# Kernel optimization log

Measured on AMD Instinct MI355X. Metric: run time of the kernel, lower is better.

Reference implementation:

```python
import jax, jax.numpy as jnp
import numpy as np

B, TQ, TK, D, H = 2, 2048, 2048, 1024, 16


def setup_inputs() -> dict:
    key = jax.random.key(0)
    ks = jax.random.split(key, 8)
    s = 1.0 / np.sqrt(D)
    x_q = jax.random.normal(ks[0], (B, TQ, D), jnp.float32)
    x_k = jax.random.normal(ks[1], (B, TK, D), jnp.float32)
    x_v = jax.random.normal(ks[2], (B, TK, D), jnp.float32)
    # causal mask, True = masked (matches masked_fill semantics)
    causal = jnp.triu(jnp.ones((TQ, TK), jnp.bool_), k=1)
    attn_mask = jnp.broadcast_to(causal, (B, TQ, TK))
    Wq = jax.random.normal(ks[3], (D, D), jnp.float32) * s
    Wk = jax.random.normal(ks[4], (D, D), jnp.float32) * s
    Wv = jax.random.normal(ks[5], (D, D), jnp.float32) * s
    Wo = jax.random.normal(ks[6], (D, D), jnp.float32) * s
    z = jnp.zeros((D,), jnp.float32)
    return {"x_q": x_q, "x_k": x_k, "x_v": x_v, "attn_mask": attn_mask,
            "Wq": Wq, "bq": z, "Wk": Wk, "bk": z, "Wv": Wv, "bv": z,
            "Wo": Wo, "bo": z, "n_heads": H}


def reference(x_q, x_k, x_v, attn_mask, Wq, bq, Wk, bk, Wv, bv, Wo, bo, n_heads):
    Bv, Tq, Dm = x_q.shape
    Tk = x_k.shape[1]
    dh = Dm // n_heads
    # nn.Linear: y = x @ W^T + b; split heads -> [B, H, T, dh]
    Q = (jnp.einsum('btd,od->bto', x_q, Wq) + bq).reshape(Bv, Tq, n_heads, dh).transpose(0, 2, 1, 3)
    K = (jnp.einsum('btd,od->bto', x_k, Wk) + bk).reshape(Bv, Tk, n_heads, dh).transpose(0, 2, 1, 3)
    V = (jnp.einsum('btd,od->bto', x_v, Wv) + bv).reshape(Bv, Tk, n_heads, dh).transpose(0, 2, 1, 3)
    scale = 1.0 / np.sqrt(dh).astype(np.float32)
    scores = jnp.einsum('bhqd,bhkd->bhqk', Q, K) * scale  # [B,H,Tq,Tk]
    scores = jnp.where(attn_mask[:, None, :, :], -jnp.inf, scores)
    A = jax.nn.softmax(scores, axis=-1)  # dropout p=0.0 -> identity
    out = jnp.einsum('bhqk,bhkd->bhqd', A, V)
    out = out.transpose(0, 2, 1, 3).reshape(Bv, Tq, Dm)
    return jnp.einsum('btd,od->bto', out, Wo) + bo
```

## Files before the change

### kernel.cpp

```cpp
#include <hip/hip_runtime.h>


typedef __attribute__((ext_vector_type(8))) __bf16 bf16x8;
typedef __attribute__((ext_vector_type(4))) float f32x4;
typedef unsigned short u16;

constexpr int BATCH  = 2;
constexpr int TSEQ   = 2048;
constexpr int DMODEL = 1024;
constexpr int NHEAD  = 16;
constexpr int DHEAD  = 64;
constexpr int MROWS  = BATCH * TSEQ;

static __device__ __forceinline__ u16 f2bf(float f) {
  union { float f; unsigned int u; } v; v.f = f;
  unsigned int u = v.u;
  return (u16)((u + 0x7fffu + ((u >> 16) & 1u)) >> 16);
}

static __device__ __forceinline__ void gload16(const void* g, void* l) {
  __builtin_amdgcn_global_load_lds(
      (const __attribute__((address_space(1))) void*)g,
      (__attribute__((address_space(3))) void*)l, 16, 0, 0);
}

__global__ __launch_bounds__(256) void cvt_multi(const float* __restrict__ s0,
                                                 const float* __restrict__ s1,
                                                 const float* __restrict__ s2,
                                                 const float* __restrict__ s3,
                                                 u16* __restrict__ d0, u16* __restrict__ d1,
                                                 u16* __restrict__ d2, u16* __restrict__ d3,
                                                 int n4) {
  const float* s; u16* d;
  switch (blockIdx.y) {
    case 0: s = s0; d = d0; break;
    case 1: s = s1; d = d1; break;
    case 2: s = s2; d = d2; break;
    default: s = s3; d = d3; break;
  }
  int i = blockIdx.x * 256 + threadIdx.x;
  if (i >= n4) return;
  float4 f = ((const float4*)s)[i];
  ushort4 o;
  o.x = f2bf(f.x); o.y = f2bf(f.y); o.z = f2bf(f.z); o.w = f2bf(f.w);
  ((ushort4*)d)[i] = o;
}

template <typename Epi>
static __device__ __forceinline__ void gemm_body8(const u16* __restrict__ X_,
                                                  const u16* __restrict__ W_,
                                                  const float* __restrict__ bias,
                                                  Epi epi) {
  __shared__ __align__(16) u16 As[2][4096];
  __shared__ __align__(16) u16 Bs[2][4096];
  const int lane = threadIdx.x & 63, wave = threadIdx.x >> 6;
  const int l16 = lane & 15, lk = lane >> 4;
  const int wm = wave >> 2, wn = wave & 3;
  const int row0 = blockIdx.x * 128, col0 = blockIdx.y * 128;
  constexpr int K = DMODEL;
  const u16* ga = X_ + (size_t)(row0 + wave * 16 + l16) * K + lk * 8;
  const u16* gb = W_ + (size_t)(col0 + wave * 16 + l16) * K + lk * 8;
  f32x4 acc[4][2];
#pragma unroll
  for (int mt = 0; mt < 4; ++mt)
#pragma unroll
    for (int nt = 0; nt < 2; ++nt) acc[mt][nt] = (f32x4){0.f, 0.f, 0.f, 0.f};
  gload16(ga, &As[0][wave * 512]);
  gload16(gb, &Bs[0][wave * 512]);
  __syncthreads();
  int buf = 0;
  for (int ks = 0; ks < K / 32; ++ks) {
    if (ks + 1 < K / 32) {
      gload16(ga + (ks + 1) * 32, &As[buf ^ 1][wave * 512]);
      gload16(gb + (ks + 1) * 32, &Bs[buf ^ 1][wave * 512]);
    }
    bf16x8 a[4], b[2];
#pragma unroll
    for (int mt = 0; mt < 4; ++mt)
      a[mt] = *(const bf16x8*)&As[buf][(wm * 4 + mt) * 512 + lane * 8];
#pragma unroll
    for (int nt = 0; nt < 2; ++nt)
      b[nt] = *(const bf16x8*)&Bs[buf][(wn * 2 + nt) * 512 + lane * 8];
#pragma unroll
    for (int mt = 0; mt < 4; ++mt)
#pragma unroll
      for (int nt = 0; nt < 2; ++nt)
        acc[mt][nt] =
            __builtin_amdgcn_mfma_f32_16x16x32_bf16(a[mt], b[nt], acc[mt][nt], 0, 0, 0);
    __syncthreads();
    buf ^= 1;
  }
#pragma unroll
  for (int mt = 0; mt < 4; ++mt)
#pragma unroll
    for (int nt = 0; nt < 2; ++nt)
#pragma unroll
      for (int r = 0; r < 4; ++r) {
        int m = row0 + wm * 64 + mt * 16 + lk * 4 + r;
        int n = col0 + wn * 32 + nt * 16 + l16;
        float v = acc[mt][nt][r] + bias[n];
        epi(m, n, v);
      }
}

template <typename Epi>
static __device__ __forceinline__ void gemm_body4(const u16* __restrict__ X_,
                                                  const u16* __restrict__ W_,
                                                  const float* __restrict__ bias,
                                                  Epi epi) {
  constexpr int K = DMODEL;
  __shared__ __align__(16) u16 As[2][8 * 512];
  __shared__ __align__(16) u16 Bs[2][4 * 512];
  const int lane = threadIdx.x & 63, wave = threadIdx.x >> 6;
  const int l16 = lane & 15, lk = lane >> 4;
  const int wm = wave >> 1, wn = wave & 1;
  const int row0 = blockIdx.x * 128, col0 = blockIdx.y * 64;
  const u16* ga = X_ + (size_t)(row0 + l16) * K + lk * 8;
  const u16* gb = W_ + (size_t)(col0 + l16) * K + lk * 8;
  f32x4 acc[4][2];
#pragma unroll
  for (int mt = 0; mt < 4; ++mt)
#pragma unroll
    for (int nt = 0; nt < 2; ++nt) acc[mt][nt] = (f32x4){0.f, 0.f, 0.f, 0.f};
  auto stage = [&](int bufi, int ks) {
#pragma unroll
    for (int j = 0; j < 2; ++j) {
      int s = j * 4 + wave;
      gload16(ga + (size_t)s * 16 * K + ks * 32, &As[bufi][s * 512]);
    }
    gload16(gb + (size_t)wave * 16 * K + ks * 32, &Bs[bufi][wave * 512]);
  };
  stage(0, 0);
  __syncthreads();
  int buf = 0;
  for (int ks = 0; ks < K / 32; ++ks) {
    if (ks + 1 < K / 32) stage(buf ^ 1, ks + 1);
    bf16x8 a[4], b[2];
#pragma unroll
    for (int mt = 0; mt < 4; ++mt)
      a[mt] = *(const bf16x8*)&As[buf][(wm * 4 + mt) * 512 + lane * 8];
#pragma unroll
    for (int nt = 0; nt < 2; ++nt)
      b[nt] = *(const bf16x8*)&Bs[buf][(wn * 2 + nt) * 512 + lane * 8];
#pragma unroll
    for (int mt = 0; mt < 4; ++mt)
#pragma unroll
      for (int nt = 0; nt < 2; ++nt)
        acc[mt][nt] =
            __builtin_amdgcn_mfma_f32_16x16x32_bf16(a[mt], b[nt], acc[mt][nt], 0, 0, 0);
    __syncthreads();
    buf ^= 1;
  }
#pragma unroll
  for (int mt = 0; mt < 4; ++mt)
#pragma unroll
    for (int nt = 0; nt < 2; ++nt)
#pragma unroll
      for (int r = 0; r < 4; ++r) {
        int m = row0 + wm * 64 + mt * 16 + lk * 4 + r;
        int n = col0 + wn * 32 + nt * 16 + l16;
        float v = acc[mt][nt][r] + bias[n];
        epi(m, n, v);
      }
}

__global__ __launch_bounds__(512) void gemm_qkv(
    const u16* __restrict__ xq, const u16* __restrict__ xk, const u16* __restrict__ xv,
    const u16* __restrict__ wq, const u16* __restrict__ wk, const u16* __restrict__ wv,
    const float* __restrict__ bq, const float* __restrict__ bk, const float* __restrict__ bv,
    u16* __restrict__ Qh, u16* __restrict__ Kh, u16* __restrict__ Vt) {
  const int z = blockIdx.z;
  const u16* X = z == 0 ? xq : (z == 1 ? xk : xv);
  const u16* W = z == 0 ? wq : (z == 1 ? wk : wv);
  const float* bias = z == 0 ? bq : (z == 1 ? bk : bv);
  u16* O01 = z == 0 ? Qh : Kh;
  gemm_body8(X, W, bias, [&](int m, int n, float v) {
    int bb = m >> 11, t = m & (TSEQ - 1);
    int h = n >> 6, dd = n & (DHEAD - 1);
    if (z == 0) v *= 0.18033688011112042f;
    if (z == 2)
      Vt[(((size_t)(bb * NHEAD + h)) * DHEAD + dd) * TSEQ + t] = f2bf(v);
    else
      O01[(((size_t)(bb * NHEAD + h)) * TSEQ + t) * DHEAD + dd] = f2bf(v);
  });
}

__global__ __launch_bounds__(256, 4) void gemm_o(const u16* __restrict__ AO,
                                                 const u16* __restrict__ wo,
                                                 const float* __restrict__ bias,
                                                 float* __restrict__ out) {
  gemm_body4(AO, wo, bias,
             [&](int m, int n, float v) { out[(size_t)m * DMODEL + n] = v; });
}

__global__ __launch_bounds__(512, 6) void flash_attn(const u16* __restrict__ Qh,
                                                     const u16* __restrict__ Kh,
                                                     const u16* __restrict__ Vt,
                                                     u16* __restrict__ AO) {
  const int lane = threadIdx.x & 63, wave = threadIdx.x >> 6;
  const int l16 = lane & 15, lk = lane >> 4;
  const int bh = blockIdx.x;
  const int qt = (gridDim.y - 1) - blockIdx.y;
  const int q0 = qt * 128;
  const int b = bh >> 4, h = bh & 15;

  __shared__ __align__(16) u16 Kl[2][4096];
  __shared__ __align__(16) u16 Vl[2][4096];
  __shared__ __align__(16) u16 plds[8][16][72];

  const u16* Qb = Qh + (size_t)bh * TSEQ * DHEAD;
  const u16* Kb = Kh + (size_t)bh * TSEQ * DHEAD;
  const u16* Vb = Vt + (size_t)bh * DHEAD * TSEQ;

  bf16x8 qf[2];
  {
    const u16* qp = Qb + (size_t)(q0 + wave * 16 + l16) * DHEAD + lk * 8;
    qf[0] = *(const bf16x8*)(qp);
    qf[1] = *(const bf16x8*)(qp + 32);
  }

  float mrow[4], lsum[4];
  f32x4 acco[4];
#pragma unroll
  for (int r = 0; r < 4; ++r) { mrow[r] = -1e30f; lsum[r] = 0.f; }
#pragma unroll
  for (int dt = 0; dt < 4; ++dt) acco[dt] = (f32x4){0.f, 0.f, 0.f, 0.f};

  auto stage_kv = [&](int bufi, int kbase) {
    int trow = (wave >> 1) * 16 + l16;
    int dhs = (wave & 1) * 4 + lk;
    gload16(Kb + (size_t)(kbase + trow) * DHEAD + dhs * 8, &Kl[bufi][wave * 512]);
    gload16(Vb + (size_t)trow * TSEQ + kbase + dhs * 8, &Vl[bufi][wave * 512]);
  };

  const int nkb = 2 * qt + 2;
  const int kbdiag = 2 * qt + (wave >> 2);
  stage_kv(0, 0);
  __syncthreads();
  int buf = 0;
  const int qrow_base = q0 + wave * 16 + 4 * lk;

  for (int kb = 0; kb < nkb; ++kb) {
    const int kbase = kb * 64;
    if (kb + 1 < nkb) stage_kv(buf ^ 1, kbase + 64);

    if (kb <= kbdiag) {
      f32x4 s[4];
#pragma unroll
      for (int nt = 0; nt < 4; ++nt) {
        bf16x8 k0f = *(const bf16x8*)&Kl[buf][nt * 1024 + lane * 8];
        bf16x8 k1f = *(const bf16x8*)&Kl[buf][nt * 1024 + 512 + lane * 8];
        f32x4 z = (f32x4){0.f, 0.f, 0.f, 0.f};
        z = __builtin_amdgcn_mfma_f32_16x16x32_bf16(qf[0], k0f, z, 0, 0, 0);
        z = __builtin_amdgcn_mfma_f32_16x16x32_bf16(qf[1], k1f, z, 0, 0, 0);
        s[nt] = z;
      }
      if (kb == kbdiag) {
#pragma unroll
        for (int nt = 0; nt < 4; ++nt)
#pragma unroll
          for (int r = 0; r < 4; ++r) {
            int kcol = kbase + nt * 16 + l16;
            s[nt][r] = (kcol <= qrow_base + r) ? s[nt][r] : -1e30f;
          }
      }
      float pmax[4];
      bool need = false;
#pragma unroll
      for (int r = 0; r < 4; ++r) {
        pmax[r] = fmaxf(fmaxf(s[0][r], s[1][r]), fmaxf(s[2][r], s[3][r]));
        need |= (pmax[r] > mrow[r] + 12.f);
      }
      if (__any(need)) {
#pragma unroll
        for (int r = 0; r < 4; ++r) {
          float mx = pmax[r];
#pragma unroll
          for (int off = 1; off < 16; off <<= 1) mx = fmaxf(mx, __shfl_xor(mx, off, 16));
          float mnew = fmaxf(mrow[r], mx);
          float alpha = exp2f(mrow[r] - mnew);
          lsum[r] *= alpha;
#pragma unroll
          for (int dt = 0; dt < 4; ++dt) acco[dt][r] *= alpha;
          mrow[r] = mnew;
        }
      }
#pragma unroll
      for (int r = 0; r < 4; ++r)
#pragma unroll
        for (int nt = 0; nt < 4; ++nt) {
          float p = exp2f(s[nt][r] - mrow[r]);
          s[nt][r] = p;
          lsum[r] += p;
        }
#pragma unroll
      for (int nt = 0; nt < 4; ++nt)
#pragma unroll
        for (int r = 0; r < 4; ++r)
          plds[wave][4 * lk + r][nt * 16 + l16] = f2bf(s[nt][r]);
      bf16x8 pf0 = *(const bf16x8*)&plds[wave][l16][lk * 8];
      bf16x8 pf1 = *(const bf16x8*)&plds[wave][l16][32 + lk * 8];
#pragma unroll
      for (int dt = 0; dt < 4; ++dt) {
        bf16x8 v0 = *(const bf16x8*)&Vl[buf][dt * 1024 + lane * 8];
        bf16x8 v1 = *(const bf16x8*)&Vl[buf][dt * 1024 + 512 + lane * 8];
        acco[dt] = __builtin_amdgcn_mfma_f32_16x16x32_bf16(pf0, v0, acco[dt], 0, 0, 0);
        acco[dt] = __builtin_amdgcn_mfma_f32_16x16x32_bf16(pf1, v1, acco[dt], 0, 0, 0);
      }
    }
    __syncthreads();
    buf ^= 1;
  }

#pragma unroll
  for (int r = 0; r < 4; ++r) {
    float t = lsum[r];
#pragma unroll
    for (int off = 1; off < 16; off <<= 1) t += __shfl_xor(t, off, 16);
    lsum[r] = 1.f / t;
  }
#pragma unroll
  for (int dt = 0; dt < 4; ++dt)
#pragma unroll
    for (int r = 0; r < 4; ++r) {
      int t = qrow_base + r;
      int col = h * DHEAD + dt * 16 + l16;
      AO[((size_t)(b * TSEQ + t)) * DMODEL + col] = f2bf(acco[dt][r] * lsum[r]);
    }
}

extern "C" void kernel_launch(void* const* d_in, const int* in_sizes, int n_in,
                              void* d_out, int out_size, void* d_ws, size_t ws_size,
                              hipStream_t stream) {
  const float* x_q = (const float*)d_in[0];
  const float* x_k = (const float*)d_in[1];
  const float* x_v = (const float*)d_in[2];
  const float* Wq = (const float*)d_in[4];
  const float* bq = (const float*)d_in[5];
  const float* Wk = (const float*)d_in[6];
  const float* bk = (const float*)d_in[7];
  const float* Wv = (const float*)d_in[8];
  const float* bv = (const float*)d_in[9];
  const float* Wo = (const float*)d_in[10];
  const float* bo = (const float*)d_in[11];

  const size_t nx = (size_t)MROWS * DMODEL;
  const size_t nw = (size_t)DMODEL * DMODEL;
  u16* ws   = (u16*)d_ws;
  u16* xq_b = ws;
  u16* xk_b = xq_b + nx;
  u16* xv_b = xk_b + nx;
  u16* wq_b = xv_b + nx;
  u16* wk_b = wq_b + nw;
  u16* wv_b = wk_b + nw;
  u16* wo_b = wv_b + nw;
  u16* Qh   = wo_b + nw;
  u16* Kh   = Qh + nx;
  u16* Vt   = Kh + nx;
  u16* AO   = Vt + nx;

  const int n4x = (int)(nx / 4), n4w = (int)(nw / 4);
  cvt_multi<<<dim3((n4x + 255) / 256, 3), 256, 0, stream>>>(
      x_q, x_k, x_v, nullptr, xq_b, xk_b, xv_b, nullptr, n4x);
  cvt_multi<<<dim3((n4w + 255) / 256, 4), 256, 0, stream>>>(
      Wq, Wk, Wv, Wo, wq_b, wk_b, wv_b, wo_b, n4w);

  gemm_qkv<<<dim3(MROWS / 128, DMODEL / 128, 3), 512, 0, stream>>>(
      xq_b, xk_b, xv_b, wq_b, wk_b, wv_b, bq, bk, bv, Qh, Kh, Vt);

  flash_attn<<<dim3(BATCH * NHEAD, TSEQ / 128), 512, 0, stream>>>(Qh, Kh, Vt, AO);

  gemm_o<<<dim3(MROWS / 128, DMODEL / 64), 256, 0, stream>>>(AO, wo_b, bo, (float*)d_out);
}
```

Before: 171.6 us.

## Pair causal q-tiles per block for balanced flash attention work

Reworks flash attention so each 4-wave block processes two 64-row query tiles (31-p and p), giving every block the same number of key-block iterations under the causal mask. This replaces the 8-wave 128-row tiles, whose per-block work varied with position and which left half the waves idle on the diagonal block. It trades a larger K/V staging cost per wave and an extra pipeline restart for better load balance and smaller blocks.

```diff
diff --git a/kernel.cpp b/kernel.cpp
--- a/kernel.cpp
+++ b/kernel.cpp
@@ -193,58 +193,60 @@
              [&](int m, int n, float v) { out[(size_t)m * DMODEL + n] = v; });
 }
 
-__global__ __launch_bounds__(512, 6) void flash_attn(const u16* __restrict__ Qh,
-                                                     const u16* __restrict__ Kh,
-                                                     const u16* __restrict__ Vt,
-                                                     u16* __restrict__ AO) {
+__global__ __launch_bounds__(256) void flash_attn(const u16* __restrict__ Qh,
+                                                  const u16* __restrict__ Kh,
+                                                  const u16* __restrict__ Vt,
+                                                  u16* __restrict__ AO) {
   const int lane = threadIdx.x & 63, wave = threadIdx.x >> 6;
   const int l16 = lane & 15, lk = lane >> 4;
   const int bh = blockIdx.x;
-  const int qt = (gridDim.y - 1) - blockIdx.y;
-  const int q0 = qt * 128;
+  const int p = blockIdx.y;
   const int b = bh >> 4, h = bh & 15;
 
   __shared__ __align__(16) u16 Kl[2][4096];
   __shared__ __align__(16) u16 Vl[2][4096];
-  __shared__ __align__(16) u16 plds[8][16][72];
+  __shared__ __align__(16) u16 plds[4][16][72];
 
   const u16* Qb = Qh + (size_t)bh * TSEQ * DHEAD;
   const u16* Kb = Kh + (size_t)bh * TSEQ * DHEAD;
   const u16* Vb = Vt + (size_t)bh * DHEAD * TSEQ;
 
-  bf16x8 qf[2];
-  {
-    const u16* qp = Qb + (size_t)(q0 + wave * 16 + l16) * DHEAD + lk * 8;
-    qf[0] = *(const bf16x8*)(qp);
-    qf[1] = *(const bf16x8*)(qp + 32);
-  }
-
-  float mrow[4], lsum[4];
-  f32x4 acco[4];
-#pragma unroll
-  for (int r = 0; r < 4; ++r) { mrow[r] = -1e30f; lsum[r] = 0.f; }
-#pragma unroll
-  for (int dt = 0; dt < 4; ++dt) acco[dt] = (f32x4){0.f, 0.f, 0.f, 0.f};
-
   auto stage_kv = [&](int bufi, int kbase) {
-    int trow = (wave >> 1) * 16 + l16;
-    int dhs = (wave & 1) * 4 + lk;
-    gload16(Kb + (size_t)(kbase + trow) * DHEAD + dhs * 8, &Kl[bufi][wave * 512]);
-    gload16(Vb + (size_t)trow * TSEQ + kbase + dhs * 8, &Vl[bufi][wave * 512]);
+#pragma unroll
+    for (int j = 0; j < 2; ++j) {
+      int s = j * 4 + wave;
+      int trow = (s >> 1) * 16 + l16;
+      int dhs = (s & 1) * 4 + lk;
+      gload16(Kb + (size_t)(kbase + trow) * DHEAD + dhs * 8, &Kl[bufi][s * 512]);
+      gload16(Vb + (size_t)trow * TSEQ + kbase + dhs * 8, &Vl[bufi][s * 512]);
+    }
   };
 
-  const int nkb = 2 * qt + 2;
-  const int kbdiag = 2 * qt + (wave >> 2);
-  stage_kv(0, 0);
-  __syncthreads();
-  int buf = 0;
-  const int qrow_base = q0 + wave * 16 + 4 * lk;
-
-  for (int kb = 0; kb < nkb; ++kb) {
-    const int kbase = kb * 64;
-    if (kb + 1 < nkb) stage_kv(buf ^ 1, kbase + 64);
-
-    if (kb <= kbdiag) {
+  auto run_tile = [&](int qt) {
+    const int q0 = qt * 64;
+    bf16x8 qf[2];
+    {
+      const u16* qp = Qb + (size_t)(q0 + wave * 16 + l16) * DHEAD + lk * 8;
+      qf[0] = *(const bf16x8*)(qp);
+      qf[1] = *(const bf16x8*)(qp + 32);
+    }
+    float mrow[4], lsum[4];
+    f32x4 acco[4];
+#pragma unroll
+    for (int r = 0; r < 4; ++r) { mrow[r] = -1e30f; lsum[r] = 0.f; }
+#pragma unroll
+    for (int dt = 0; dt < 4; ++dt) acco[dt] = (f32x4){0.f, 0.f, 0.f, 0.f};
+
+    const int qrow_base = q0 + wave * 16 + 4 * lk;
+    const int nkb = qt + 1;
+    stage_kv(0, 0);
+    __syncthreads();
+    int buf = 0;
+
+    for (int kb = 0; kb < nkb; ++kb) {
+      const int kbase = kb * 64;
+      if (kb + 1 < nkb) stage_kv(buf ^ 1, kbase + 64);
+
       f32x4 s[4];
 #pragma unroll
       for (int nt = 0; nt < 4; ++nt) {
@@ -255,7 +257,7 @@
         z = __builtin_amdgcn_mfma_f32_16x16x32_bf16(qf[1], k1f, z, 0, 0, 0);
         s[nt] = z;
       }
-      if (kb == kbdiag) {
+      if (kb == qt) {
 #pragma unroll
         for (int nt = 0; nt < 4; ++nt)
 #pragma unroll
@@ -289,9 +291,9 @@
       for (int r = 0; r < 4; ++r)
 #pragma unroll
         for (int nt = 0; nt < 4; ++nt) {
-          float p = exp2f(s[nt][r] - mrow[r]);
-          s[nt][r] = p;
-          lsum[r] += p;
+          float pv = exp2f(s[nt][r] - mrow[r]);
+          s[nt][r] = pv;
+          lsum[r] += pv;
         }
 #pragma unroll
       for (int nt = 0; nt < 4; ++nt)
@@ -307,26 +309,29 @@
         acco[dt] = __builtin_amdgcn_mfma_f32_16x16x32_bf16(pf0, v0, acco[dt], 0, 0, 0);
         acco[dt] = __builtin_amdgcn_mfma_f32_16x16x32_bf16(pf1, v1, acco[dt], 0, 0, 0);
       }
-    }
-    __syncthreads();
-    buf ^= 1;
-  }
-
-#pragma unroll
-  for (int r = 0; r < 4; ++r) {
-    float t = lsum[r];
-#pragma unroll
-    for (int off = 1; off < 16; off <<= 1) t += __shfl_xor(t, off, 16);
-    lsum[r] = 1.f / t;
-  }
-#pragma unroll
-  for (int dt = 0; dt < 4; ++dt)
+      __syncthreads();
+      buf ^= 1;
+    }
+
 #pragma unroll
     for (int r = 0; r < 4; ++r) {
-      int t = qrow_base + r;
-      int col = h * DHEAD + dt * 16 + l16;
-      AO[((size_t)(b * TSEQ + t)) * DMODEL + col] = f2bf(acco[dt][r] * lsum[r]);
-    }
+      float t = lsum[r];
+#pragma unroll
+      for (int off = 1; off < 16; off <<= 1) t += __shfl_xor(t, off, 16);
+      lsum[r] = 1.f / t;
+    }
+#pragma unroll
+    for (int dt = 0; dt < 4; ++dt)
+#pragma unroll
+      for (int r = 0; r < 4; ++r) {
+        int t = qrow_base + r;
+        int col = h * DHEAD + dt * 16 + l16;
+        AO[((size_t)(b * TSEQ + t)) * DMODEL + col] = f2bf(acco[dt][r] * lsum[r]);
+      }
+  };
+
+  run_tile(31 - p);
+  run_tile(p);
 }
 
 extern "C" void kernel_launch(void* const* d_in, const int* in_sizes, int n_in,
@@ -368,7 +373,7 @@
   gemm_qkv<<<dim3(MROWS / 128, DMODEL / 128, 3), 512, 0, stream>>>(
       xq_b, xk_b, xv_b, wq_b, wk_b, wv_b, bq, bk, bv, Qh, Kh, Vt);
 
-  flash_attn<<<dim3(BATCH * NHEAD, TSEQ / 128), 512, 0, stream>>>(Qh, Kh, Vt, AO);
+  flash_attn<<<dim3(BATCH * NHEAD, TSEQ / 128), 256, 0, stream>>>(Qh, Kh, Vt, AO);
 
   gemm_o<<<dim3(MROWS / 128, DMODEL / 64), 256, 0, stream>>>(AO, wo_b, bo, (float*)d_out);
 }
```

Result: faster. 166.9 us (-2.7%).
